# Kernel optimization log

Hardware: AMD Instinct MI355X
Metric: run time of the kernel (lower is better)

The kernel has to match this reference:

```python
import jax, jax.numpy as jnp
import numpy as np

FORGET_RADIX = 10
HIDDEN_RADIX = 23
LN2 = float(np.log(2.0))
MAX_FORGET = 0.875
BATCH, IN_SIZE, H_SIZE = 8192, 1024, 2048
G = H_SIZE // 2  # group size (h_size // 2)


def setup_inputs() -> dict:
    key = jax.random.key(0)
    ks = jax.random.split(key, 6)
    x = jax.random.normal(ks[0], (BATCH, IN_SIZE), dtype=jnp.float32)
    # hidden is a fixed-point (radix 23) int state; values correspond to floats in (-0.125, 0.125)
    hidden = jax.random.randint(ks[1], (BATCH, H_SIZE), -(2**20), 2**20, dtype=jnp.int32)

    def lin(k, fan_in, fan_out):
        kw, kb = jax.random.split(k)
        s = 1.0 / np.sqrt(fan_in)
        W = jax.random.uniform(kw, (fan_in, fan_out), jnp.float32, -s, s)
        b = jax.random.uniform(kb, (fan_out,), jnp.float32, -s, s)
        return W, b

    W_zr1, b_zr1 = lin(ks[2], IN_SIZE + G, H_SIZE)
    W_g1, b_g1 = lin(ks[3], IN_SIZE + G, G)
    W_zr2, b_zr2 = lin(ks[4], IN_SIZE + G, H_SIZE)
    W_g2, b_g2 = lin(ks[5], IN_SIZE + G, G)
    return {"x": x, "hidden": hidden,
            "W_zr1": W_zr1, "b_zr1": b_zr1, "W_g1": W_g1, "b_g1": b_g1,
            "W_zr2": W_zr2, "b_zr2": b_zr2, "W_g2": W_g2, "b_g2": b_g2,
            "slice_dim": 0}


def _to_float(h_fix, radix):
    # ConvertToFloat: fixed-point int -> float
    return h_fix.astype(jnp.float32) / np.float32(2.0 ** radix)


def _to_fixed(v, radix):
    # ConvertToFixed: float -> fixed-point int (truncation toward zero, like Tensor.int())
    return jnp.trunc(v * np.float32(2.0 ** radix)).astype(jnp.int64)


def reference(x, hidden, W_zr1, b_zr1, W_g1, b_g1, W_zr2, b_zr2, W_g2, b_g2, slice_dim):
    h = hidden.astype(jnp.int64)  # widen so h * z_fix (up to ~2^34) does not overflow
    h1, h2 = h[:, :G], h[:, G:]

    # ---- group 1 update (reads h2) ----
    h2_fl = _to_float(h2, HIDDEN_RADIX)
    zr1 = jax.nn.sigmoid(jnp.concatenate([x, h2_fl], axis=1) @ W_zr1 + b_zr1)
    z1, r1 = zr1[:, :G], zr1[:, G:]
    z1 = MAX_FORGET * z1 + (1.0 - MAX_FORGET)
    g1 = jnp.tanh(jnp.concatenate([x, r1 * h2_fl], axis=1) @ W_g1 + b_g1)
    z1_fix = jnp.maximum(_to_fixed(z1, FORGET_RADIX), 1)  # EnsureNotForgetAll
    h1 = jnp.floor_divide(h1 * z1_fix, 2 ** FORGET_RADIX)  # FixedMultiply, buf=None, mask=1
    h1 = h1 + _to_fixed((1.0 - z1) * g1, HIDDEN_RADIX)     # + MaskFixedMultiply(update1, 1)

    # ---- group 2 update (reads updated h1) ----
    h1_fl = _to_float(h1, HIDDEN_RADIX)
    zr2 = jax.nn.sigmoid(jnp.concatenate([x, h1_fl], axis=1) @ W_zr2 + b_zr2)
    z2, r2 = zr2[:, :G], zr2[:, G:]
    z2 = MAX_FORGET * z2 + (1.0 - MAX_FORGET)
    g2 = jnp.tanh(jnp.concatenate([x, r2 * h1_fl], axis=1) @ W_g2 + b_g2)
    z2_fix = jnp.maximum(_to_fixed(z2, FORGET_RADIX), 1)
    h2 = jnp.floor_divide(h2 * z2_fix, 2 ** FORGET_RADIX)
    h2 = h2 + _to_fixed((1.0 - z2) * g2, HIDDEN_RADIX)

    recurrent_hidden = jnp.concatenate([h1, h2], axis=1).astype(jnp.int32)
    output_hidden = recurrent_hidden.astype(jnp.float32) / np.float32(2.0 ** HIDDEN_RADIX)

    optimal_bits = (jnp.sum(-jnp.log(z1[:, slice_dim:]) / LN2)
                    + jnp.sum(-jnp.log(z2) / LN2)
                    + 32.0 * slice_dim * x.shape[0])
    return recurrent_hidden, output_hidden, optimal_bits
```

## Files before the change

kernel.cpp:

```cpp
#include <hip/hip_runtime.h>
#include <hip/hip_bf16.h>

#define BATCH   8192
#define IN_SZ   1024
#define HSZ     2048
#define GG      1024
#define KTOT    2048

typedef __hip_bfloat16 bf16;
typedef __attribute__((ext_vector_type(8))) short  short8;
typedef __attribute__((ext_vector_type(4))) float  floatx4;

typedef __attribute__((address_space(1))) const void gvoid_t;
typedef __attribute__((address_space(3))) void       lvoid_t;

__device__ __forceinline__ void async_ld16(void* lds, const void* g) {
  __builtin_amdgcn_global_load_lds((gvoid_t*)g, (lvoid_t*)lds, 16, 0, 0);
}

__global__ void prep_all(const float* __restrict__ x, bf16* __restrict__ xb,
                         const int* __restrict__ hidden, bf16* __restrict__ hf,
                         float* accp,
                         const float* __restrict__ W_zr1, const float* __restrict__ W_g1,
                         const float* __restrict__ W_zr2, const float* __restrict__ W_g2,
                         bf16* __restrict__ wt_zr1, bf16* __restrict__ wt_g1,
                         bf16* __restrict__ wt_zr2, bf16* __restrict__ wt_g2) {
  int b = blockIdx.x;
  int t = threadIdx.x;
  if (b < 3072) {
    const float* W; bf16* Wt; int N; int tb = b;
    if (tb < 1024)      { W = W_zr1; Wt = wt_zr1; N = 2048; }
    else if (tb < 1536) { W = W_g1;  Wt = wt_g1;  N = 1024; tb -= 1024; }
    else if (tb < 2560) { W = W_zr2; Wt = wt_zr2; N = 2048; tb -= 1536; }
    else                { W = W_g2;  Wt = wt_g2;  N = 1024; tb -= 2560; }
    int ntn = N >> 6;
    int k0 = (tb / ntn) * 64, n0 = (tb % ntn) * 64;
    __shared__ float tile[64][65];
    int kk = t >> 4, nn = (t & 15) * 4;
#pragma unroll
    for (int s = 0; s < 4; ++s) {
      int row = kk + s * 16;
      float4 v = *(const float4*)&W[(size_t)(k0 + row) * N + n0 + nn];
      tile[row][nn + 0] = v.x; tile[row][nn + 1] = v.y;
      tile[row][nn + 2] = v.z; tile[row][nn + 3] = v.w;
    }
    __syncthreads();
    int k8 = (t & 7) * 8;
#pragma unroll
    for (int s = 0; s < 2; ++s) {
      int nl = (t >> 3) + s * 32;
      bf16 vals[8];
#pragma unroll
      for (int u = 0; u < 8; ++u) vals[u] = __float2bfloat16(tile[k8 + u][nl]);
      *(short8*)&Wt[(size_t)(n0 + nl) * KTOT + k0 + k8] = *(short8*)vals;
    }
  } else {
    int idx = (b - 3072) * 256 + t;
    int i = idx * 4;
    float4 xv = *(const float4*)(x + i);
    xb[i + 0] = __float2bfloat16(xv.x);
    xb[i + 1] = __float2bfloat16(xv.y);
    xb[i + 2] = __float2bfloat16(xv.z);
    xb[i + 3] = __float2bfloat16(xv.w);
    int m = i >> 10, j = i & 1023;
    int4 hv = *(const int4*)(hidden + m * HSZ + GG + j);
    const float sc = 1.0f / 8388608.0f;
    hf[i + 0] = __float2bfloat16((float)hv.x * sc);
    hf[i + 1] = __float2bfloat16((float)hv.y * sc);
    hf[i + 2] = __float2bfloat16((float)hv.z * sc);
    hf[i + 3] = __float2bfloat16((float)hv.w * sc);
    if (idx == 0) *accp = 0.0f;
  }
}

template<int BM, int BN, int MI, int NJ>
__device__ __forceinline__ void gemm_mainloop(const bf16* __restrict__ Aleft,
                                              const bf16* __restrict__ Aright,
                                              const bf16* __restrict__ Bt,
                                              bf16* As, bf16* Bs,
                                              int m0, int n0, floatx4 (&acc)[MI][NJ]) {
  constexpr int ACALLS = BM / 32;
  constexpr int BCALLS = BN / 32;
  int t = threadIdx.x;
  int lane = t & 63;
  int w = t >> 6;
  int l3 = lane >> 3;
  int gchunk = (lane & 7) ^ l3;
  int rbase = w * 8 + l3;
  int q = lane >> 4, r16 = lane & 15;
  int wm = w & 1, wn = w >> 1;

  size_t a_off[ACALLS], b_off[BCALLS];
  bf16 *lA[ACALLS], *lB[BCALLS];
#pragma unroll
  for (int s = 0; s < ACALLS; ++s) {
    a_off[s] = (size_t)(m0 + rbase + s * 32) * IN_SZ + gchunk * 8;
    lA[s] = As + (s * 32 + w * 8) * 64 + lane * 8;
  }
#pragma unroll
  for (int s = 0; s < BCALLS; ++s) {
    b_off[s] = (size_t)(n0 + rbase + s * 32) * KTOT + gchunk * 8;
    lB[s] = Bs + (s * 32 + w * 8) * 64 + lane * 8;
  }
  const bf16* aRdBase = As + (wm * (BM / 2) + r16) * 64;
  const bf16* bRdBase = Bs + (wn * (BN / 2) + r16) * 64;
  int pc[2];
  pc[0] = ((q) ^ (r16 & 7)) * 8;
  pc[1] = ((4 + q) ^ (r16 & 7)) * 8;

  for (int kb = 0; kb < KTOT / 64; ++kb) {
    int kt = kb * 64;
    const bf16* asrc; int kloc;
    if (kt < IN_SZ) { asrc = Aleft;  kloc = kt; }
    else            { asrc = Aright; kloc = kt - IN_SZ; }
#pragma unroll
    for (int s = 0; s < ACALLS; ++s) async_ld16(lA[s], asrc + a_off[s] + kloc);
#pragma unroll
    for (int s = 0; s < BCALLS; ++s) async_ld16(lB[s], Bt + b_off[s] + kt);
    __syncthreads();
#pragma unroll
    for (int kh = 0; kh < 2; ++kh) {
      short8 af[MI], bfr[NJ];
#pragma unroll
      for (int i = 0; i < MI; ++i)
        af[i]  = *(const short8*)(const void*)(aRdBase + i * 16 * 64 + pc[kh]);
#pragma unroll
      for (int j = 0; j < NJ; ++j)
        bfr[j] = *(const short8*)(const void*)(bRdBase + j * 16 * 64 + pc[kh]);
#pragma unroll
      for (int i = 0; i < MI; ++i)
#pragma unroll
        for (int j = 0; j < NJ; ++j)
          acc[i][j] = __builtin_amdgcn_mfma_f32_16x16x32_bf16(af[i], bfr[j], acc[i][j], 0, 0, 0);
    }
    __syncthreads();
  }
}

__global__ void __launch_bounds__(256, 4)
gemm_zr(const bf16* __restrict__ xb, const bf16* __restrict__ hfp,
        const bf16* __restrict__ Bt, const float* __restrict__ bias,
        bf16* __restrict__ zbuf, bf16* __restrict__ rh,
        const int* __restrict__ slice_ptr, int use_slice,
        float* __restrict__ accp) {
  __shared__ bf16 As[128 * 64];
  __shared__ bf16 Bs[128 * 64];
  floatx4 acc[4][4];
#pragma unroll
  for (int i = 0; i < 4; ++i)
#pragma unroll
    for (int j = 0; j < 4; ++j) acc[i][j] = (floatx4)0.0f;

  int linear = blockIdx.y * gridDim.x + blockIdx.x;
  int m0 = (linear & 63) * 128, n0 = (linear >> 6) * 128;
  gemm_mainloop<128, 128, 4, 4>(xb, hfp, Bt, As, Bs, m0, n0, acc);

  int t = threadIdx.x;
  int lane = t & 63, q = lane >> 4, r16 = lane & 15;
  int w = t >> 6, wm = w & 1, wn = w >> 1;
  int nmin = use_slice ? *slice_ptr : 0;
  float lsum = 0.0f;

#pragma unroll
  for (int i = 0; i < 4; ++i) {
    int mbase = m0 + wm * 64 + i * 16 + q * 4;
#pragma unroll
    for (int j = 0; j < 4; ++j) {
      int n = n0 + wn * 64 + j * 16 + r16;
      float bn = bias[n];
#pragma unroll
      for (int rr = 0; rr < 4; ++rr) {
        int m = mbase + rr;
        float v = acc[i][j][rr] + bn;
        float s = 1.0f / (1.0f + __expf(-v));
        if (n < GG) {
          float z = 0.875f * s + 0.125f;
          zbuf[(size_t)m * GG + n] = __float2bfloat16(z);
          if (n >= nmin) lsum += -__log2f(z);
        } else {
          int jc = n - GG;
          float hfl = __bfloat162float(hfp[(size_t)m * GG + jc]);
          rh[(size_t)m * GG + jc] = __float2bfloat16(s * hfl);
        }
      }
    }
  }
  __syncthreads();
  float* sf = (float*)As;
#pragma unroll
  for (int off = 32; off > 0; off >>= 1) lsum += __shfl_down(lsum, off, 64);
  if (lane == 0) sf[w] = lsum;
  __syncthreads();
  if (t == 0) atomicAdd(accp, sf[0] + sf[1] + sf[2] + sf[3]);
}

__global__ void __launch_bounds__(256, 4)
gemm_g(const bf16* __restrict__ xb, const bf16* __restrict__ rh,
       const bf16* __restrict__ Bt, const float* __restrict__ bias,
       const bf16* __restrict__ zbuf, const int* __restrict__ hidden,
       int col_off,
       float* __restrict__ out0, float* __restrict__ out1,
       bf16* __restrict__ hf_out, int write_hf,
       int write_bits, const float* __restrict__ accp,
       const int* __restrict__ slice_ptr, float* __restrict__ out2) {
  __shared__ bf16 As[128 * 64];
  __shared__ bf16 Bs[64 * 64];
  floatx4 acc[4][2];
#pragma unroll
  for (int i = 0; i < 4; ++i)
#pragma unroll
    for (int j = 0; j < 2; ++j) acc[i][j] = (floatx4)0.0f;

  int linear = blockIdx.y * gridDim.x + blockIdx.x;
  int m0 = (linear & 63) * 128, n0 = (linear >> 6) * 64;
  gemm_mainloop<128, 64, 4, 2>(xb, rh, Bt, As, Bs, m0, n0, acc);

  int t = threadIdx.x;
  int lane = t & 63, q = lane >> 4, r16 = lane & 15;
  int w = t >> 6, wm = w & 1, wn = w >> 1;

#pragma unroll
  for (int i = 0; i < 4; ++i) {
    int mbase = m0 + wm * 64 + i * 16 + q * 4;
#pragma unroll
    for (int j = 0; j < 2; ++j) {
      int n = n0 + wn * 32 + j * 16 + r16;
      float bn = bias[n];
#pragma unroll
      for (int rr = 0; rr < 4; ++rr) {
        int m = mbase + rr;
        float v = acc[i][j][rr] + bn;
        float e = __expf(2.0f * v);
        float g = 1.0f - 2.0f / (e + 1.0f);
        float z = __bfloat162float(zbuf[(size_t)m * GG + n]);
        int zfix = (int)(z * 1024.0f);
        if (zfix < 1) zfix = 1;
        long long h = hidden[(size_t)m * HSZ + col_off + n];
        long long hupd = (h * (long long)zfix) >> 10;
        float t2 = (1.0f - z) * g * 8388608.0f;
        long long f2 = (long long)t2;
        int hnew = (int)(hupd + f2);
        size_t oidx = (size_t)m * HSZ + col_off + n;
        out0[oidx] = (float)hnew;
        float ofl = (float)hnew * (1.0f / 8388608.0f);
        out1[oidx] = ofl;
        if (write_hf) hf_out[(size_t)m * GG + n] = __float2bfloat16(ofl);
      }
    }
  }
  if (write_bits && blockIdx.x == 0 && blockIdx.y == 0 && t == 0) {
    *out2 = *accp + 32.0f * (float)(*slice_ptr) * (float)BATCH;
  }
}

extern "C" void kernel_launch(void* const* d_in, const int* in_sizes, int n_in,
                              void* d_out, int out_size, void* d_ws, size_t ws_size,
                              hipStream_t stream) {
  const float* x      = (const float*)d_in[0];
  const int*   hidden = (const int*)d_in[1];
  const float* W_zr1  = (const float*)d_in[2];
  const float* b_zr1  = (const float*)d_in[3];
  const float* W_g1   = (const float*)d_in[4];
  const float* b_g1   = (const float*)d_in[5];
  const float* W_zr2  = (const float*)d_in[6];
  const float* b_zr2  = (const float*)d_in[7];
  const float* W_g2   = (const float*)d_in[8];
  const float* b_g2   = (const float*)d_in[9];
  const int*   slice  = (const int*)d_in[10];

  char* ws = (char*)d_ws;
  size_t off = 0;
  auto alloc = [&](size_t bytes) -> void* {
    void* p = ws + off;
    off += (bytes + 255) & ~(size_t)255;
    return p;
  };
  bf16* xb     = (bf16*)alloc((size_t)BATCH * IN_SZ * 2);
  bf16* wt_zr1 = (bf16*)alloc((size_t)2048 * 2048 * 2);
  bf16* wt_g1  = (bf16*)alloc((size_t)1024 * 2048 * 2);
  bf16* wt_zr2 = (bf16*)alloc((size_t)2048 * 2048 * 2);
  bf16* wt_g2  = (bf16*)alloc((size_t)1024 * 2048 * 2);
  bf16* hf     = (bf16*)alloc((size_t)BATCH * GG * 2);
  bf16* rh     = (bf16*)alloc((size_t)BATCH * GG * 2);
  bf16* zbuf   = (bf16*)alloc((size_t)BATCH * GG * 2);
  float* accp  = (float*)alloc(256);

  float* out0 = (float*)d_out;
  float* out1 = out0 + (size_t)BATCH * HSZ;
  float* out2 = out0 + 2 * (size_t)BATCH * HSZ;

  prep_all<<<3072 + 8192, 256, 0, stream>>>(x, xb, hidden, hf, accp,
                                            W_zr1, W_g1, W_zr2, W_g2,
                                            wt_zr1, wt_g1, wt_zr2, wt_g2);

  gemm_zr<<<dim3(16, 64), 256, 0, stream>>>(xb, hf, wt_zr1, b_zr1, zbuf, rh, slice, 1, accp);
  gemm_g<<<dim3(16, 64), 256, 0, stream>>>(xb, rh, wt_g1, b_g1, zbuf, hidden, 0,
                                           out0, out1, hf, 1, 0, accp, slice, out2);
  gemm_zr<<<dim3(16, 64), 256, 0, stream>>>(xb, hf, wt_zr2, b_zr2, zbuf, rh, slice, 0, accp);
  gemm_g<<<dim3(16, 64), 256, 0, stream>>>(xb, rh, wt_g2, b_g2, zbuf, hidden, 1024,
                                           out0, out1, hf, 0, 1, accp, slice, out2);
}
```

Before: 578.5 us.

## Rewrite GEMMs as 8-wave 256-row tiles with double-buffered phased pipeline and LDS epilogue

Replaces the 4-wave 128x128/128x64 GEMM kernels with 512-thread blocks computing 256x256 (zr) and 256x128 (g) tiles. The main loop double-buffers A/B in 128KB of LDS and splits each k-step into quadrant phases that interleave async global->LDS loads with MFMA work, using raw s_barrier, waitcnt and setprio. Epilogues stage results through swizzled LDS so global stores and loads become 4-wide and coalesced. The larger tiles reduce redundant operand traffic, at the cost of fewer, larger blocks (256 per GEMM, with 2 allowed per CU by the launch bounds), heavy register pressure and fragile hand-tuned wait counts.

```diff
diff --git a/kernel.cpp b/kernel.cpp
--- a/kernel.cpp
+++ b/kernel.cpp
@@ -9,6 +9,7 @@
 
 typedef __hip_bfloat16 bf16;
 typedef __attribute__((ext_vector_type(8))) short  short8;
+typedef __attribute__((ext_vector_type(4))) short  short4e;
 typedef __attribute__((ext_vector_type(4))) float  floatx4;
 
 typedef __attribute__((address_space(1))) const void gvoid_t;
@@ -73,184 +74,302 @@
   }
 }
 
-template<int BM, int BN, int MI, int NJ>
-__device__ __forceinline__ void gemm_mainloop(const bf16* __restrict__ Aleft,
-                                              const bf16* __restrict__ Aright,
-                                              const bf16* __restrict__ Bt,
-                                              bf16* As, bf16* Bs,
-                                              int m0, int n0, floatx4 (&acc)[MI][NJ]) {
-  constexpr int ACALLS = BM / 32;
-  constexpr int BCALLS = BN / 32;
-  int t = threadIdx.x;
-  int lane = t & 63;
-  int w = t >> 6;
-  int l3 = lane >> 3;
-  int gchunk = (lane & 7) ^ l3;
-  int rbase = w * 8 + l3;
-  int q = lane >> 4, r16 = lane & 15;
-  int wm = w & 1, wn = w >> 1;
-
-  size_t a_off[ACALLS], b_off[BCALLS];
-  bf16 *lA[ACALLS], *lB[BCALLS];
-#pragma unroll
-  for (int s = 0; s < ACALLS; ++s) {
-    a_off[s] = (size_t)(m0 + rbase + s * 32) * IN_SZ + gchunk * 8;
-    lA[s] = As + (s * 32 + w * 8) * 64 + lane * 8;
+
+#define BAR() asm volatile("s_barrier" ::: "memory")
+
+#define DS_A(buf, qm) do {                                                   \
+  _Pragma("unroll") for (int ii = 0; ii < 4; ++ii) {                         \
+    const bf16* _ap = As + (buf)*16384 + (wm*128 + (qm)*64 + ii*16 + r16)*64;\
+    af[ii][0] = *(const short8*)(const void*)(_ap + pcq0);                   \
+    af[ii][1] = *(const short8*)(const void*)(_ap + pcq1);                   \
+  } } while (0)
+
+#define DS_B(buf, qn) do {                                                   \
+  _Pragma("unroll") for (int jj = 0; jj < NJQ; ++jj) {                       \
+    const int _brow = (BN == 256) ? (wn*64 + (qn)*32 + jj*16 + r16)          \
+                                  : (wn*32 + (qn)*16 + r16);                 \
+    const bf16* _bp = Bs + (buf)*BSTR + _brow*64;                            \
+    bfr[jj][0] = *(const short8*)(const void*)(_bp + pcq0);                  \
+    bfr[jj][1] = *(const short8*)(const void*)(_bp + pcq1);                  \
+  } } while (0)
+
+#define MFMA_Q(qm, qn) do {                                                  \
+  _Pragma("unroll") for (int ii = 0; ii < 4; ++ii)                           \
+  _Pragma("unroll") for (int jj = 0; jj < NJQ; ++jj) {                       \
+    floatx4& _c = acc[(qm)*4 + ii][(qn)*NJQ + jj];                           \
+    _c = __builtin_amdgcn_mfma_f32_16x16x32_bf16(af[ii][0], bfr[jj][0], _c, 0, 0, 0); \
+    _c = __builtin_amdgcn_mfma_f32_16x16x32_bf16(af[ii][1], bfr[jj][1], _c, 0, 0, 0); \
+  } } while (0)
+
+#define STAGE_A(buf, qm, tk) do {                                            \
+  const int _t = (tk);                                                       \
+  const bf16* _p = (_t < 16 ? A0 : A1);                                      \
+  const int _k = ((_t & 15) << 6) + gch8;                                    \
+  async_ld16(As + (buf)*16384 + (qm)*4096 + w*512 + lnoff,        _p + a_sro[qm][0] + _k); \
+  async_ld16(As + (buf)*16384 + 8192 + (qm)*4096 + w*512 + lnoff, _p + a_sro[qm][1] + _k); \
+} while (0)
+
+#define STAGE_B(buf, qn, tk) do {                                            \
+  const int _k = ((tk) << 6) + gch8;                                         \
+  if constexpr (BN == 256) {                                                 \
+    async_ld16(Bs + (buf)*BSTR + ((w>>2)*64 + (qn)*32 + (w&3)*8)*64 + lnoff,       Bt + b_sro[qn][0] + _k); \
+    async_ld16(Bs + (buf)*BSTR + (128 + (w>>2)*64 + (qn)*32 + (w&3)*8)*64 + lnoff, Bt + b_sro[qn][1] + _k); \
+  } else {                                                                   \
+    async_ld16(Bs + (buf)*BSTR + ((w>>1)*32 + (qn)*16 + (w&1)*8)*64 + lnoff,       Bt + b_sro[qn][0] + _k); \
+  }                                                                          \
+} while (0)
+
+#define PHASE(buf, qm, qn, NEWA, STAGE_STMT, DOVM) do {                      \
+  if (NEWA) DS_A(buf, qm);                                                   \
+  DS_B(buf, qn);                                                             \
+  STAGE_STMT;                                                                \
+  BAR();                                                                     \
+  asm volatile("s_waitcnt lgkmcnt(0)" ::: "memory");                         \
+  __builtin_amdgcn_sched_barrier(0);                                         \
+  __builtin_amdgcn_s_setprio(1);                                             \
+  MFMA_Q(qm, qn);                                                            \
+  __builtin_amdgcn_s_setprio(0);                                             \
+  if (DOVM) { if constexpr (BN == 256) asm volatile("s_waitcnt vmcnt(4)" ::: "memory"); \
+              else                     asm volatile("s_waitcnt vmcnt(3)" ::: "memory"); } \
+  BAR();                                                                     \
+} while (0)
+
+template<int BN>
+__device__ __forceinline__ void mainloop8(const bf16* __restrict__ A0,
+                                          const bf16* __restrict__ A1,
+                                          const bf16* __restrict__ Bt,
+                                          bf16* As, bf16* Bs,
+                                          int m0, int n0,
+                                          floatx4 (&acc)[8][BN / 64]) {
+  constexpr int NJQ  = BN / 128;
+  constexpr int BSTR = BN * 64;
+  const int t    = threadIdx.x;
+  const int lane = t & 63;
+  const int w    = t >> 6;
+  const int l3   = lane >> 3;
+  const int gch8 = (((lane & 7) ^ l3) << 3);
+  const int lnoff = lane << 3;
+  const int wm = w & 1, wn = w >> 1;
+  const int q = lane >> 4, r16 = lane & 15;
+  const int pcq0 = ((q)     ^ (r16 & 7)) << 3;
+  const int pcq1 = ((4 + q) ^ (r16 & 7)) << 3;
+
+  int a_sro[2][2], b_sro[2][2];
+#pragma unroll
+  for (int qm = 0; qm < 2; ++qm)
+#pragma unroll
+    for (int h = 0; h < 2; ++h)
+      a_sro[qm][h] = (m0 + h*128 + qm*64 + w*8 + l3) * 1024;
+#pragma unroll
+  for (int qn = 0; qn < 2; ++qn) {
+    if constexpr (BN == 256) {
+#pragma unroll
+      for (int h = 0; h < 2; ++h)
+        b_sro[qn][h] = (n0 + h*128 + (w>>2)*64 + qn*32 + (w&3)*8 + l3) * KTOT;
+    } else {
+      b_sro[qn][0] = (n0 + (w>>1)*32 + qn*16 + (w&1)*8 + l3) * KTOT;
+      b_sro[qn][1] = 0;
+    }
   }
-#pragma unroll
-  for (int s = 0; s < BCALLS; ++s) {
-    b_off[s] = (size_t)(n0 + rbase + s * 32) * KTOT + gchunk * 8;
-    lB[s] = Bs + (s * 32 + w * 8) * 64 + lane * 8;
+
+  STAGE_A(0, 0, 0); STAGE_B(0, 0, 0);
+  STAGE_A(0, 1, 0); STAGE_B(0, 1, 0);
+  STAGE_A(1, 0, 1); STAGE_B(1, 0, 1);
+  if constexpr (BN == 256) asm volatile("s_waitcnt vmcnt(4)" ::: "memory");
+  else                     asm volatile("s_waitcnt vmcnt(3)" ::: "memory");
+  BAR();
+
+#pragma unroll 1
+  for (int it = 0; it < KTOT / 128; ++it) {
+    const int tO = 2*it + 1;
+    const int t2 = (2*it + 2 < KTOT/64) ? (2*it + 2) : (KTOT/64 - 1);
+    const int t3 = (2*it + 3 < KTOT/64) ? (2*it + 3) : (KTOT/64 - 1);
+    short8 af[4][2];
+    short8 bfr[NJQ][2];
+    PHASE(0, 0, 0, 1, STAGE_A(1, 1, tO), 0);
+    PHASE(0, 0, 1, 0, STAGE_B(1, 1, tO), 0);
+    PHASE(0, 1, 0, 1, STAGE_A(0, 0, t2), 0);
+    PHASE(0, 1, 1, 0, STAGE_B(0, 0, t2), 1);
+    PHASE(1, 0, 0, 1, STAGE_A(0, 1, t2), 0);
+    PHASE(1, 0, 1, 0, STAGE_B(0, 1, t2), 0);
+    PHASE(1, 1, 0, 1, STAGE_A(1, 0, t3), 0);
+    PHASE(1, 1, 1, 0, STAGE_B(1, 0, t3), 1);
   }
-  const bf16* aRdBase = As + (wm * (BM / 2) + r16) * 64;
-  const bf16* bRdBase = Bs + (wn * (BN / 2) + r16) * 64;
-  int pc[2];
-  pc[0] = ((q) ^ (r16 & 7)) * 8;
-  pc[1] = ((4 + q) ^ (r16 & 7)) * 8;
-
-  for (int kb = 0; kb < KTOT / 64; ++kb) {
-    int kt = kb * 64;
-    const bf16* asrc; int kloc;
-    if (kt < IN_SZ) { asrc = Aleft;  kloc = kt; }
-    else            { asrc = Aright; kloc = kt - IN_SZ; }
-#pragma unroll
-    for (int s = 0; s < ACALLS; ++s) async_ld16(lA[s], asrc + a_off[s] + kloc);
-#pragma unroll
-    for (int s = 0; s < BCALLS; ++s) async_ld16(lB[s], Bt + b_off[s] + kt);
+  asm volatile("s_waitcnt vmcnt(0)" ::: "memory");
+  __syncthreads();
+}
+
+__global__ void __launch_bounds__(512, 2)
+gemm_zr8(const bf16* __restrict__ xb, const bf16* __restrict__ hfp,
+         const bf16* __restrict__ Bt, const float* __restrict__ bias,
+         bf16* __restrict__ zbuf, bf16* __restrict__ rh,
+         const int* __restrict__ slice_ptr, int use_slice,
+         float* __restrict__ accp) {
+  __shared__ __attribute__((aligned(16))) char smem[131072];
+  bf16* As = (bf16*)smem;
+  bf16* Bs = (bf16*)(smem + 65536);
+  const int m0 = blockIdx.y * 256;
+  const int n0 = blockIdx.x * 256;
+  floatx4 acc[8][4];
+#pragma unroll
+  for (int i = 0; i < 8; ++i)
+#pragma unroll
+    for (int j = 0; j < 4; ++j) acc[i][j] = (floatx4)0.0f;
+
+  mainloop8<256>(xb, hfp, Bt, As, Bs, m0, n0, acc);
+
+  const int t = threadIdx.x;
+  const int lane = t & 63, w = t >> 6;
+  const int wm = w & 1, wn = w >> 1;
+  const int q = lane >> 4, r16 = lane & 15;
+  float* lds_f = (float*)smem;
+  const bool zmode = (n0 < GG);
+  const int nmin = use_slice ? *slice_ptr : 0;
+  float bn[4];
+#pragma unroll
+  for (int j = 0; j < 4; ++j) bn[j] = bias[n0 + wn*64 + j*16 + r16];
+  float lsum = 0.0f;
+
+#pragma unroll
+  for (int p = 0; p < 2; ++p) {
+#pragma unroll
+    for (int i4 = 0; i4 < 4; ++i4)
+#pragma unroll
+      for (int j = 0; j < 4; ++j) {
+        const int n_loc = wn*64 + j*16 + r16;
+        const int n = n0 + n_loc;
+#pragma unroll
+        for (int rr = 0; rr < 4; ++rr) {
+          const int lr = wm*64 + i4*16 + q*4 + rr;
+          float v = acc[p*4 + i4][j][rr] + bn[j];
+          float s = 1.0f / (1.0f + __expf(-v));
+          float ov;
+          if (zmode) {
+            float z = 0.875f * s + 0.125f;
+            if (n >= nmin) lsum += -__log2f(z);
+            ov = z;
+          } else {
+            ov = s;
+          }
+          lds_f[lr*256 + ((((n_loc >> 2) ^ (lr & 7)) << 2) | (n_loc & 3))] = ov;
+        }
+      }
     __syncthreads();
 #pragma unroll
-    for (int kh = 0; kh < 2; ++kh) {
-      short8 af[MI], bfr[NJ];
-#pragma unroll
-      for (int i = 0; i < MI; ++i)
-        af[i]  = *(const short8*)(const void*)(aRdBase + i * 16 * 64 + pc[kh]);
-#pragma unroll
-      for (int j = 0; j < NJ; ++j)
-        bfr[j] = *(const short8*)(const void*)(bRdBase + j * 16 * 64 + pc[kh]);
-#pragma unroll
-      for (int i = 0; i < MI; ++i)
-#pragma unroll
-        for (int j = 0; j < NJ; ++j)
-          acc[i][j] = __builtin_amdgcn_mfma_f32_16x16x32_bf16(af[i], bfr[j], acc[i][j], 0, 0, 0);
+    for (int s2 = 0; s2 < 16; ++s2) {
+      const int r = w*16 + s2;
+      const int c = lane;
+      floatx4 v4 = *(const floatx4*)&lds_f[r*256 + ((c ^ (r & 7)) << 2)];
+      const int m = m0 + (r >> 6)*128 + p*64 + (r & 63);
+      const int ncol = n0 + c*4;
+      if (zmode) {
+        bf16 o[4];
+#pragma unroll
+        for (int e = 0; e < 4; ++e) o[e] = __float2bfloat16(v4[e]);
+        *(short4e*)&zbuf[(size_t)m * GG + ncol] = *(short4e*)o;
+      } else {
+        const int jc = ncol - GG;
+        short4e hv = *(const short4e*)&hfp[(size_t)m * GG + jc];
+        bf16 o[4];
+#pragma unroll
+        for (int e = 0; e < 4; ++e) {
+          float hfv = __uint_as_float((unsigned)(unsigned short)hv[e] << 16);
+          o[e] = __float2bfloat16(v4[e] * hfv);
+        }
+        *(short4e*)&rh[(size_t)m * GG + jc] = *(short4e*)o;
+      }
     }
     __syncthreads();
   }
-}
-
-__global__ void __launch_bounds__(256, 4)
-gemm_zr(const bf16* __restrict__ xb, const bf16* __restrict__ hfp,
-        const bf16* __restrict__ Bt, const float* __restrict__ bias,
-        bf16* __restrict__ zbuf, bf16* __restrict__ rh,
-        const int* __restrict__ slice_ptr, int use_slice,
-        float* __restrict__ accp) {
-  __shared__ bf16 As[128 * 64];
-  __shared__ bf16 Bs[128 * 64];
-  floatx4 acc[4][4];
-#pragma unroll
-  for (int i = 0; i < 4; ++i)
-#pragma unroll
-    for (int j = 0; j < 4; ++j) acc[i][j] = (floatx4)0.0f;
-
-  int linear = blockIdx.y * gridDim.x + blockIdx.x;
-  int m0 = (linear & 63) * 128, n0 = (linear >> 6) * 128;
-  gemm_mainloop<128, 128, 4, 4>(xb, hfp, Bt, As, Bs, m0, n0, acc);
-
-  int t = threadIdx.x;
-  int lane = t & 63, q = lane >> 4, r16 = lane & 15;
-  int w = t >> 6, wm = w & 1, wn = w >> 1;
-  int nmin = use_slice ? *slice_ptr : 0;
-  float lsum = 0.0f;
-
-#pragma unroll
-  for (int i = 0; i < 4; ++i) {
-    int mbase = m0 + wm * 64 + i * 16 + q * 4;
-#pragma unroll
-    for (int j = 0; j < 4; ++j) {
-      int n = n0 + wn * 64 + j * 16 + r16;
-      float bn = bias[n];
-#pragma unroll
-      for (int rr = 0; rr < 4; ++rr) {
-        int m = mbase + rr;
-        float v = acc[i][j][rr] + bn;
-        float s = 1.0f / (1.0f + __expf(-v));
-        if (n < GG) {
-          float z = 0.875f * s + 0.125f;
-          zbuf[(size_t)m * GG + n] = __float2bfloat16(z);
-          if (n >= nmin) lsum += -__log2f(z);
-        } else {
-          int jc = n - GG;
-          float hfl = __bfloat162float(hfp[(size_t)m * GG + jc]);
-          rh[(size_t)m * GG + jc] = __float2bfloat16(s * hfl);
-        }
-      }
-    }
-  }
-  __syncthreads();
-  float* sf = (float*)As;
 #pragma unroll
   for (int off = 32; off > 0; off >>= 1) lsum += __shfl_down(lsum, off, 64);
+  float* sf = (float*)smem;
   if (lane == 0) sf[w] = lsum;
   __syncthreads();
-  if (t == 0) atomicAdd(accp, sf[0] + sf[1] + sf[2] + sf[3]);
-}
-
-__global__ void __launch_bounds__(256, 4)
-gemm_g(const bf16* __restrict__ xb, const bf16* __restrict__ rh,
-       const bf16* __restrict__ Bt, const float* __restrict__ bias,
-       const bf16* __restrict__ zbuf, const int* __restrict__ hidden,
-       int col_off,
-       float* __restrict__ out0, float* __restrict__ out1,
-       bf16* __restrict__ hf_out, int write_hf,
-       int write_bits, const float* __restrict__ accp,
-       const int* __restrict__ slice_ptr, float* __restrict__ out2) {
-  __shared__ bf16 As[128 * 64];
-  __shared__ bf16 Bs[64 * 64];
-  floatx4 acc[4][2];
-#pragma unroll
-  for (int i = 0; i < 4; ++i)
+  if (t == 0)
+    atomicAdd(accp, sf[0]+sf[1]+sf[2]+sf[3]+sf[4]+sf[5]+sf[6]+sf[7]);
+}
+
+__global__ void __launch_bounds__(512, 2)
+gemm_g8(const bf16* __restrict__ xb, const bf16* __restrict__ rh,
+        const bf16* __restrict__ Bt, const float* __restrict__ bias,
+        const bf16* __restrict__ zbuf, const int* __restrict__ hidden,
+        int col_off,
+        float* __restrict__ out0, float* __restrict__ out1,
+        bf16* __restrict__ hf_out, int write_hf,
+        int write_bits, const float* __restrict__ accp,
+        const int* __restrict__ slice_ptr, float* __restrict__ out2) {
+  __shared__ __attribute__((aligned(16))) char smem[131072];
+  bf16* As = (bf16*)smem;
+  bf16* Bs = (bf16*)(smem + 65536);
+  const int m0 = blockIdx.y * 256;
+  const int n0 = blockIdx.x * 128;
+  floatx4 acc[8][2];
+#pragma unroll
+  for (int i = 0; i < 8; ++i)
 #pragma unroll
     for (int j = 0; j < 2; ++j) acc[i][j] = (floatx4)0.0f;
 
-  int linear = blockIdx.y * gridDim.x + blockIdx.x;
-  int m0 = (linear & 63) * 128, n0 = (linear >> 6) * 64;
-  gemm_mainloop<128, 64, 4, 2>(xb, rh, Bt, As, Bs, m0, n0, acc);
-
-  int t = threadIdx.x;
-  int lane = t & 63, q = lane >> 4, r16 = lane & 15;
-  int w = t >> 6, wm = w & 1, wn = w >> 1;
-
-#pragma unroll
-  for (int i = 0; i < 4; ++i) {
-    int mbase = m0 + wm * 64 + i * 16 + q * 4;
+  mainloop8<128>(xb, rh, Bt, As, Bs, m0, n0, acc);
+
+  const int t = threadIdx.x;
+  const int lane = t & 63, w = t >> 6;
+  const int wm = w & 1, wn = w >> 1;
+  const int q = lane >> 4, r16 = lane & 15;
+  float* lds_f = (float*)smem;
+  float bn[2];
+#pragma unroll
+  for (int j = 0; j < 2; ++j) bn[j] = bias[n0 + wn*32 + j*16 + r16];
+
+#pragma unroll
+  for (int i = 0; i < 8; ++i)
 #pragma unroll
     for (int j = 0; j < 2; ++j) {
-      int n = n0 + wn * 32 + j * 16 + r16;
-      float bn = bias[n];
+      const int n_loc = wn*32 + j*16 + r16;
 #pragma unroll
       for (int rr = 0; rr < 4; ++rr) {
-        int m = mbase + rr;
-        float v = acc[i][j][rr] + bn;
-        float e = __expf(2.0f * v);
-        float g = 1.0f - 2.0f / (e + 1.0f);
-        float z = __bfloat162float(zbuf[(size_t)m * GG + n]);
-        int zfix = (int)(z * 1024.0f);
-        if (zfix < 1) zfix = 1;
-        long long h = hidden[(size_t)m * HSZ + col_off + n];
-        long long hupd = (h * (long long)zfix) >> 10;
-        float t2 = (1.0f - z) * g * 8388608.0f;
-        long long f2 = (long long)t2;
-        int hnew = (int)(hupd + f2);
-        size_t oidx = (size_t)m * HSZ + col_off + n;
-        out0[oidx] = (float)hnew;
-        float ofl = (float)hnew * (1.0f / 8388608.0f);
-        out1[oidx] = ofl;
-        if (write_hf) hf_out[(size_t)m * GG + n] = __float2bfloat16(ofl);
+        const int lr = wm*128 + i*16 + q*4 + rr;
+        lds_f[lr*128 + ((((n_loc >> 2) ^ (lr & 7)) << 2) | (n_loc & 3))] =
+            acc[i][j][rr] + bn[j];
       }
     }
+  __syncthreads();
+#pragma unroll
+  for (int s2 = 0; s2 < 16; ++s2) {
+    const int r = w*2 + (lane >> 5) + s2*16;
+    const int c = lane & 31;
+    floatx4 v4 = *(const floatx4*)&lds_f[r*128 + ((c ^ (r & 7)) << 2)];
+    const int m = m0 + r;
+    const int ncol = n0 + c*4;
+    short4e zb = *(const short4e*)&zbuf[(size_t)m * GG + ncol];
+    int4 hd = *(const int4*)&hidden[(size_t)m * HSZ + col_off + ncol];
+    const int hvv[4] = {hd.x, hd.y, hd.z, hd.w};
+    floatx4 w0, w1;
+    bf16 ob[4];
+#pragma unroll
+    for (int e = 0; e < 4; ++e) {
+      float v = v4[e];
+      float ex = __expf(2.0f * v);
+      float gg = 1.0f - 2.0f / (ex + 1.0f);
+      float z = __uint_as_float((unsigned)(unsigned short)zb[e] << 16);
+      int zfix = (int)(z * 1024.0f);
+      if (zfix < 1) zfix = 1;
+      long long h = hvv[e];
+      long long hupd = (h * (long long)zfix) >> 10;
+      float t2f = (1.0f - z) * gg * 8388608.0f;
+      long long f2 = (long long)t2f;
+      int hnew = (int)(hupd + f2);
+      w0[e] = (float)hnew;
+      w1[e] = (float)hnew * (1.0f / 8388608.0f);
+      ob[e] = __float2bfloat16(w1[e]);
+    }
+    const size_t ob_ = (size_t)m * HSZ + col_off + ncol;
+    *(floatx4*)&out0[ob_] = w0;
+    *(floatx4*)&out1[ob_] = w1;
+    if (write_hf) *(short4e*)&hf_out[(size_t)m * GG + ncol] = *(short4e*)ob;
   }
-  if (write_bits && blockIdx.x == 0 && blockIdx.y == 0 && t == 0) {
+  if (write_bits && blockIdx.x == 0 && blockIdx.y == 0 && t == 0)
     *out2 = *accp + 32.0f * (float)(*slice_ptr) * (float)BATCH;
-  }
 }
 
 extern "C" void kernel_launch(void* const* d_in, const int* in_sizes, int n_in,
@@ -293,10 +412,10 @@
                                             W_zr1, W_g1, W_zr2, W_g2,
                                             wt_zr1, wt_g1, wt_zr2, wt_g2);
 
-  gemm_zr<<<dim3(16, 64), 256, 0, stream>>>(xb, hf, wt_zr1, b_zr1, zbuf, rh, slice, 1, accp);
-  gemm_g<<<dim3(16, 64), 256, 0, stream>>>(xb, rh, wt_g1, b_g1, zbuf, hidden, 0,
+  gemm_zr8<<<dim3(8, 32), 512, 0, stream>>>(xb, hf, wt_zr1, b_zr1, zbuf, rh, slice, 1, accp);
+  gemm_g8<<<dim3(8, 32), 512, 0, stream>>>(xb, rh, wt_g1, b_g1, zbuf, hidden, 0,
                                            out0, out1, hf, 1, 0, accp, slice, out2);
-  gemm_zr<<<dim3(16, 64), 256, 0, stream>>>(xb, hf, wt_zr2, b_zr2, zbuf, rh, slice, 0, accp);
-  gemm_g<<<dim3(16, 64), 256, 0, stream>>>(xb, rh, wt_g2, b_g2, zbuf, hidden, 1024,
+  gemm_zr8<<<dim3(8, 32), 512, 0, stream>>>(xb, hf, wt_zr2, b_zr2, zbuf, rh, slice, 0, accp);
+  gemm_g8<<<dim3(8, 32), 512, 0, stream>>>(xb, rh, wt_g2, b_g2, zbuf, hidden, 1024,
                                            out0, out1, hf, 0, 1, accp, slice, out2);
 }
```

After: 528.3 us. -8.7%, faster.
